# Kernel optimization log

Hardware: AMD Instinct MI355X
Metric: run time of the kernel (lower is better)

## Reference

```python
import jax, jax.numpy as jnp
import numpy as np

B, L, D, H = 4, 1024, 768, 12
HD = D // H  # head_dim = 64
SCALING = HD ** -0.5


def setup_inputs() -> dict:
    key = jax.random.key(0)
    ks = jax.random.split(key, 6)
    x = jax.random.normal(ks[0], (B, L, D), dtype=jnp.float32)
    attn_bias = jax.random.normal(ks[1], (B, H, L, L), dtype=jnp.float32)
    s_in = 1.0 / np.sqrt(D)
    w_in = jax.random.uniform(ks[2], (3 * D, D), dtype=jnp.float32, minval=-s_in, maxval=s_in)
    b_in = jax.random.uniform(ks[3], (3 * D,), dtype=jnp.float32, minval=-s_in, maxval=s_in)
    w_out = jax.random.uniform(ks[4], (D, D), dtype=jnp.float32, minval=-s_in, maxval=s_in)
    b_out = jax.random.uniform(ks[5], (D,), dtype=jnp.float32, minval=-s_in, maxval=s_in)
    return {"x": x, "attn_bias": attn_bias, "w_in": w_in, "b_in": b_in,
            "w_out": w_out, "b_out": b_out}


def reference(x, attn_bias, w_in, b_in, w_out, b_out):
    # fused QKV projection: [B, L, 3D]
    qkv = jnp.einsum('bld,ed->ble', x, w_in) + b_in
    q, k, v = jnp.split(qkv, 3, axis=-1)
    # [B, H, L, HD]
    q = q.reshape(B, L, H, HD).transpose(0, 2, 1, 3) * SCALING
    k = k.reshape(B, L, H, HD).transpose(0, 2, 1, 3)
    v = v.reshape(B, L, H, HD).transpose(0, 2, 1, 3)
    # bias-augmented attention scores: [B, H, L, L]
    scores = jnp.einsum('bhqd,bhkd->bhqk', q, k) + attn_bias
    probs = jax.nn.softmax(scores, axis=-1)
    # attend: [B, H, L, HD] -> [B, L, D]
    o = jnp.einsum('bhqk,bhkd->bhqd', probs, v)
    o = o.transpose(0, 2, 1, 3).reshape(B, L, D)
    return jnp.einsum('bld,ed->ble', o, w_out) + b_out
```

## Files before the change

### kernel.cpp

```cpp
#include <hip/hip_runtime.h>
#include <hip/hip_bf16.h>
#include <stdint.h>

#define B_ 4
#define L_ 1024
#define D_ 768
#define H_ 12
#define HD_ 64
#define M_ 4096
#define N3_ 2304

typedef float f32x4 __attribute__((ext_vector_type(4)));
typedef float f32x4v __attribute__((ext_vector_type(4)));
typedef short bf16x8 __attribute__((ext_vector_type(8)));
typedef unsigned short u16;
typedef u16 u16x8 __attribute__((ext_vector_type(8)));
typedef u16 u16x4 __attribute__((ext_vector_type(4)));

#define AS3 __attribute__((address_space(3)))
#define AS1 __attribute__((address_space(1)))

__device__ __forceinline__ void gll16(const void* g, void* l) {
  __builtin_amdgcn_global_load_lds((const AS1 void*)g, (AS3 void*)l, 16, 0, 0);
}

__device__ __forceinline__ u16 f2bf(float f) {
  uint32_t u = __builtin_bit_cast(uint32_t, f);
  u += 0x7fffu + ((u >> 16) & 1u);
  return (u16)(u >> 16);
}

__global__ void k_cvt3(const float* __restrict__ a, u16* __restrict__ ao, int na4,
                       const float* __restrict__ b, u16* __restrict__ bo, int nb4,
                       const float* __restrict__ c, u16* __restrict__ co, int nc4) {
  int i = blockIdx.x * 256 + threadIdx.x;
  const float* src;
  u16* dst;
  if (i < na4) {
    src = a; dst = ao;
  } else if (i < na4 + nb4) {
    src = b; dst = bo; i -= na4;
  } else if (i < na4 + nb4 + nc4) {
    src = c; dst = co; i -= na4 + nb4;
  } else {
    return;
  }
  f32x4v v = ((const f32x4v*)src)[i];
  u16x4 o;
  o.x = f2bf(v.x); o.y = f2bf(v.y); o.z = f2bf(v.z); o.w = f2bf(v.w);
  ((u16x4*)dst)[i] = o;
}

__global__ __launch_bounds__(256) void k_gemm_qkv(
    const u16* __restrict__ Xb, const u16* __restrict__ Wb,
    const float* __restrict__ b_in,
    u16* __restrict__ gQ, u16* __restrict__ gK, u16* __restrict__ gV) {
  __shared__ u16 As[128 * 64];
  __shared__ u16 Bs[128 * 64];
  const int tid = threadIdx.x;
  const int lane = tid & 63;
  const int w = tid >> 6;
  const int wm = (w >> 1) * 64;
  const int wn = (w & 1) * 64;
  const int lr = lane & 15;
  const int lg = lane >> 4;
  const int m0 = blockIdx.x * 128;
  const int n0 = blockIdx.y * 128;

  f32x4 acc[4][4];
#pragma unroll
  for (int i = 0; i < 4; ++i)
#pragma unroll
    for (int j = 0; j < 4; ++j) acc[i][j] = (f32x4){0.f, 0.f, 0.f, 0.f};

  for (int kt = 0; kt < 12; ++kt) {
    __syncthreads();
#pragma unroll
    for (int i = 0; i < 4; ++i) {
      int seg = i * 256 + tid;
      int row = seg >> 3;
      int sl = (seg & 7) ^ (row & 7);
      gll16(Xb + (size_t)(m0 + row) * 768 + kt * 64 + sl * 8, (char*)As + seg * 16);
      gll16(Wb + (size_t)(n0 + row) * 768 + kt * 64 + sl * 8, (char*)Bs + seg * 16);
    }
    __syncthreads();
#pragma unroll
    for (int kh = 0; kh < 2; ++kh) {
      bf16x8 af[4], bfr[4];
#pragma unroll
      for (int t = 0; t < 4; ++t) {
        int ra = wm + t * 16 + lr;
        af[t] = *(const bf16x8*)((const char*)As + ra * 128 +
                                 ((kh * 64 + lg * 16) ^ ((ra & 7) << 4)));
        int rb = wn + t * 16 + lr;
        bfr[t] = *(const bf16x8*)((const char*)Bs + rb * 128 +
                                  ((kh * 64 + lg * 16) ^ ((rb & 7) << 4)));
      }
#pragma unroll
      for (int mi = 0; mi < 4; ++mi)
#pragma unroll
        for (int ni = 0; ni < 4; ++ni)
          acc[mi][ni] = __builtin_amdgcn_mfma_f32_16x16x32_bf16(
              af[mi], bfr[ni], acc[mi][ni], 0, 0, 0);
    }
  }
  const int sec = blockIdx.y / 6;
  u16* dst = sec == 0 ? gQ : (sec == 1 ? gK : gV);
  const float scale = sec == 0 ? 0.125f : 1.0f;
#pragma unroll
  for (int ni = 0; ni < 4; ++ni) {
    int e = n0 + wn + ni * 16 + lr;
    float bias = b_in[e];
    int es = e - sec * 768;
    int h = es >> 6, d = es & 63;
#pragma unroll
    for (int mi = 0; mi < 4; ++mi) {
#pragma unroll
      for (int j = 0; j < 4; ++j) {
        int m = m0 + wm + mi * 16 + lg * 4 + j;
        int bb = m >> 10, lq = m & 1023;
        float vv = (acc[mi][ni][j] + bias) * scale;
        dst[(size_t)((bb * 12 + h) * 1024 + lq) * 64 + d] = f2bf(vv);
      }
    }
  }
}

__global__ __launch_bounds__(256) void k_transpose(const u16* __restrict__ V,
                                                   u16* __restrict__ Vt) {
  __shared__ u16 t[64][66];
  const int tid = threadIdx.x;
  const int bh = blockIdx.x >> 4;
  const int kv0 = (blockIdx.x & 15) * 64;
  {
    int r = tid >> 2, c0 = (tid & 3) * 16;
    const u16* src = V + (size_t)(bh * 1024 + kv0 + r) * 64 + c0;
#pragma unroll
    for (int p = 0; p < 2; ++p) {
      u16x8 x = *(const u16x8*)(src + p * 8);
#pragma unroll
      for (int e = 0; e < 8; ++e) t[r][c0 + p * 8 + e] = x[e];
    }
  }
  __syncthreads();
  {
    int d = tid >> 2, k0 = (tid & 3) * 16;
    u16* dst = Vt + (size_t)(bh * 64 + d) * 1024 + kv0 + k0;
#pragma unroll
    for (int p = 0; p < 2; ++p) {
      u16x8 o;
#pragma unroll
      for (int e = 0; e < 8; ++e) o[e] = t[k0 + p * 8 + e][d];
      *(u16x8*)(dst + p * 8) = o;
    }
  }
}

__global__ __launch_bounds__(256) void k_attn(
    const u16* __restrict__ gQ, const u16* __restrict__ gK,
    const u16* __restrict__ gVt, const float* __restrict__ gBias,
    u16* __restrict__ gO) {
  __shared__ u16 Ks[2][64 * 64];
  __shared__ u16 Vs[2][64 * 64];
  __shared__ u16 Pl[4][16 * 64];
  const int tid = threadIdx.x;
  const int lane = tid & 63;
  const int w = tid >> 6;
  const int lr = lane & 15;
  const int lg = lane >> 4;
  const int lb = (blockIdx.x & 7) * 96 + (blockIdx.x >> 3);
  const int bh = lb >> 4;
  const int q0 = (lb & 15) * 64;
  const int qr = q0 + w * 16;

#define STAGE_KV(buf, kv0)                                                         \
  do {                                                                             \
    _Pragma("unroll") for (int i_ = 0; i_ < 2; ++i_) {                             \
      int seg_ = i_ * 256 + tid;                                                   \
      int row_ = seg_ >> 3;                                                        \
      int sl_ = (seg_ & 7) ^ (row_ & 7);                                           \
      gll16(gK + (size_t)(bh * 1024 + (kv0) + row_) * 64 + sl_ * 8,                \
            (char*)Ks[buf] + seg_ * 16);                                           \
      gll16(gVt + (size_t)(bh * 64 + row_) * 1024 + (kv0) + sl_ * 8,               \
            (char*)Vs[buf] + seg_ * 16);                                           \
    }                                                                              \
  } while (0)

  bf16x8 qa[2];
#pragma unroll
  for (int kh = 0; kh < 2; ++kh)
    qa[kh] = *(const bf16x8*)(gQ + (size_t)(bh * 1024 + qr + lr) * 64 + kh * 32 + lg * 8);

  f32x4 oacc[4];
#pragma unroll
  for (int dt = 0; dt < 4; ++dt) oacc[dt] = (f32x4){0.f, 0.f, 0.f, 0.f};
  float mrow[4] = {-1e30f, -1e30f, -1e30f, -1e30f};
  float lrow[4] = {0.f, 0.f, 0.f, 0.f};

  const float* bbase = gBias + (size_t)(bh * 1024 + qr) * 1024;

  STAGE_KV(0, 0);
  float bcur[16];
#pragma unroll
  for (int ni = 0; ni < 4; ++ni)
#pragma unroll
    for (int j = 0; j < 4; ++j)
      bcur[ni * 4 + j] = __builtin_nontemporal_load(
          bbase + (size_t)(lg * 4 + j) * 1024 + ni * 16 + lr);
  __syncthreads();

  for (int t = 0; t < 16; ++t) {
    const int cur = t & 1;
    if (t < 15) STAGE_KV(cur ^ 1, (t + 1) * 64);

    f32x4 s[4];
#pragma unroll
    for (int ni = 0; ni < 4; ++ni) s[ni] = (f32x4){0.f, 0.f, 0.f, 0.f};
    __builtin_amdgcn_s_setprio(1);
#pragma unroll
    for (int kh = 0; kh < 2; ++kh) {
#pragma unroll
      for (int ni = 0; ni < 4; ++ni) {
        int rb = ni * 16 + lr;
        bf16x8 kb = *(const bf16x8*)((const char*)Ks[cur] + rb * 128 +
                                     ((kh * 64 + lg * 16) ^ ((rb & 7) << 4)));
        s[ni] = __builtin_amdgcn_mfma_f32_16x16x32_bf16(qa[kh], kb, s[ni], 0, 0, 0);
      }
    }
    __builtin_amdgcn_s_setprio(0);

#pragma unroll
    for (int ni = 0; ni < 4; ++ni)
#pragma unroll
      for (int j = 0; j < 4; ++j) s[ni][j] += bcur[ni * 4 + j];

    float bnx[16];
    if (t < 15) {
      const float* bp = bbase + (t + 1) * 64;
#pragma unroll
      for (int ni = 0; ni < 4; ++ni)
#pragma unroll
        for (int j = 0; j < 4; ++j)
          bnx[ni * 4 + j] = __builtin_nontemporal_load(
              bp + (size_t)(lg * 4 + j) * 1024 + ni * 16 + lr);
    }

#pragma unroll
    for (int j = 0; j < 4; ++j) {
      float vm = fmaxf(fmaxf(s[0][j], s[1][j]), fmaxf(s[2][j], s[3][j]));
      vm = fmaxf(vm, __shfl_xor(vm, 1));
      vm = fmaxf(vm, __shfl_xor(vm, 2));
      vm = fmaxf(vm, __shfl_xor(vm, 4));
      vm = fmaxf(vm, __shfl_xor(vm, 8));
      float mnew = fmaxf(mrow[j], vm);
      float al = __expf(mrow[j] - mnew);
      mrow[j] = mnew;
      float rs = 0.f;
#pragma unroll
      for (int ni = 0; ni < 4; ++ni) {
        float p = __expf(s[ni][j] - mnew);
        s[ni][j] = p;
        rs += p;
      }
      rs += __shfl_xor(rs, 1);
      rs += __shfl_xor(rs, 2);
      rs += __shfl_xor(rs, 4);
      rs += __shfl_xor(rs, 8);
      lrow[j] = lrow[j] * al + rs;
#pragma unroll
      for (int dt = 0; dt < 4; ++dt) oacc[dt][j] *= al;
    }

    u16* pw = Pl[w];
#pragma unroll
    for (int ni = 0; ni < 4; ++ni)
#pragma unroll
      for (int j = 0; j < 4; ++j) {
        int row = lg * 4 + j;
        int bc = (ni * 16 + lr) * 2;
        *(u16*)((char*)pw + row * 128 + (bc ^ ((row & 7) << 4))) = f2bf(s[ni][j]);
      }
    __builtin_amdgcn_s_setprio(1);
#pragma unroll
    for (int kh = 0; kh < 2; ++kh) {
      bf16x8 pa = *(const bf16x8*)((const char*)pw + lr * 128 +
                                   ((kh * 64 + lg * 16) ^ ((lr & 7) << 4)));
#pragma unroll
      for (int dt = 0; dt < 4; ++dt) {
        int rv = dt * 16 + lr;
        bf16x8 vb = *(const bf16x8*)((const char*)Vs[cur] + rv * 128 +
                                     ((kh * 64 + lg * 16) ^ ((rv & 7) << 4)));
        oacc[dt] = __builtin_amdgcn_mfma_f32_16x16x32_bf16(pa, vb, oacc[dt], 0, 0, 0);
      }
    }
    __builtin_amdgcn_s_setprio(0);

    if (t < 15) {
#pragma unroll
      for (int z = 0; z < 16; ++z) bcur[z] = bnx[z];
    }
    __syncthreads();
  }

  const int bg = bh / 12, h = bh % 12;
#pragma unroll
  for (int j = 0; j < 4; ++j) {
    float inv = 1.0f / lrow[j];
    int row = qr + lg * 4 + j;
#pragma unroll
    for (int dt = 0; dt < 4; ++dt) {
      gO[(size_t)(bg * 1024 + row) * 768 + h * 64 + dt * 16 + lr] =
          f2bf(oacc[dt][j] * inv);
    }
  }
#undef STAGE_KV
}

__global__ __launch_bounds__(256) void k_gemm_out(
    const u16* __restrict__ Ob, const u16* __restrict__ Wb,
    const float* __restrict__ b_out, float* __restrict__ out) {
  __shared__ u16 As[128 * 64];
  __shared__ u16 Bs[128 * 64];
  const int tid = threadIdx.x;
  const int lane = tid & 63;
  const int w = tid >> 6;
  const int wm = (w >> 1) * 64;
  const int wn = (w & 1) * 64;
  const int lr = lane & 15;
  const int lg = lane >> 4;
  const int m0 = blockIdx.x * 128;
  const int n0 = blockIdx.y * 128;

  f32x4 acc[4][4];
#pragma unroll
  for (int i = 0; i < 4; ++i)
#pragma unroll
    for (int j = 0; j < 4; ++j) acc[i][j] = (f32x4){0.f, 0.f, 0.f, 0.f};

  for (int kt = 0; kt < 12; ++kt) {
    __syncthreads();
#pragma unroll
    for (int i = 0; i < 4; ++i) {
      int seg = i * 256 + tid;
      int row = seg >> 3;
      int sl = (seg & 7) ^ (row & 7);
      gll16(Ob + (size_t)(m0 + row) * 768 + kt * 64 + sl * 8, (char*)As + seg * 16);
      gll16(Wb + (size_t)(n0 + row) * 768 + kt * 64 + sl * 8, (char*)Bs + seg * 16);
    }
    __syncthreads();
#pragma unroll
    for (int kh = 0; kh < 2; ++kh) {
      bf16x8 af[4], bfr[4];
#pragma unroll
      for (int t = 0; t < 4; ++t) {
        int ra = wm + t * 16 + lr;
        af[t] = *(const bf16x8*)((const char*)As + ra * 128 +
                                 ((kh * 64 + lg * 16) ^ ((ra & 7) << 4)));
        int rb = wn + t * 16 + lr;
        bfr[t] = *(const bf16x8*)((const char*)Bs + rb * 128 +
                                  ((kh * 64 + lg * 16) ^ ((rb & 7) << 4)));
      }
#pragma unroll
      for (int mi = 0; mi < 4; ++mi)
#pragma unroll
        for (int ni = 0; ni < 4; ++ni)
          acc[mi][ni] = __builtin_amdgcn_mfma_f32_16x16x32_bf16(
              af[mi], bfr[ni], acc[mi][ni], 0, 0, 0);
    }
  }
#pragma unroll
  for (int ni = 0; ni < 4; ++ni) {
    int n = n0 + wn + ni * 16 + lr;
    float bias = b_out[n];
#pragma unroll
    for (int mi = 0; mi < 4; ++mi) {
#pragma unroll
      for (int j = 0; j < 4; ++j) {
        int m = m0 + wm + mi * 16 + lg * 4 + j;
        out[(size_t)m * 768 + n] = acc[mi][ni][j] + bias;
      }
    }
  }
}

extern "C" void kernel_launch(void* const* d_in, const int* in_sizes, int n_in,
                              void* d_out, int out_size, void* d_ws, size_t ws_size,
                              hipStream_t stream) {
  const float* x = (const float*)d_in[0];
  const float* attn_bias = (const float*)d_in[1];
  const float* w_in = (const float*)d_in[2];
  const float* b_in = (const float*)d_in[3];
  const float* w_out = (const float*)d_in[4];
  const float* b_out = (const float*)d_in[5];
  float* out = (float*)d_out;

  char* ws = (char*)d_ws;
  size_t off = 0;
  u16* xb = (u16*)(ws + off);  off += (size_t)M_ * D_ * 2;
  u16* wib = (u16*)(ws + off); off += (size_t)N3_ * D_ * 2;
  u16* wob = (u16*)(ws + off); off += (size_t)D_ * D_ * 2;
  u16* q = (u16*)(ws + off);   off += (size_t)48 * 1024 * 64 * 2;
  u16* k = (u16*)(ws + off);   off += (size_t)48 * 1024 * 64 * 2;
  u16* v = (u16*)(ws + off);   off += (size_t)48 * 1024 * 64 * 2;
  u16* vt = (u16*)(ws + off);  off += (size_t)48 * 1024 * 64 * 2;
  u16* ob = (u16*)(ws + off);  off += (size_t)M_ * D_ * 2;

  const int na4 = (M_ * D_) / 4;
  const int nb4 = (N3_ * D_) / 4;
  const int nc4 = (D_ * D_) / 4;
  k_cvt3<<<(na4 + nb4 + nc4 + 255) / 256, 256, 0, stream>>>(
      x, xb, na4, w_in, wib, nb4, w_out, wob, nc4);
  k_gemm_qkv<<<dim3(32, 18), 256, 0, stream>>>(xb, wib, b_in, q, k, v);
  k_transpose<<<768, 256, 0, stream>>>(v, vt);
  k_attn<<<768, 256, 0, stream>>>(q, k, vt, attn_bias, ob);
  k_gemm_out<<<dim3(32, 6), 256, 0, stream>>>(ob, wob, b_out, out);
}
```

Measured before the change: 130.0 us.

## Stage attention bias in LDS, read K/V directly into registers, shrink out-proj tiles

The attention kernel no longer stages K and V through shared memory. Each wave loads its K and V fragments straight from global memory into registers, and the bias tile is instead double-buffered into LDS with async global-to-LDS loads and a swizzle. The QK^T MFMA operands are swapped so each lane owns a single query row, which turns the per-row max and sum reductions into two cross-group shuffles and lets P be written to LDS as packed 32-bit stores. The output projection GEMM moves from 128x128 to 64x64 tiles to launch four times as many blocks. The costs are redundant per-wave K/V global loads, since four waves now read the same K/V tile, and lower arithmetic intensity in the output GEMM.

```diff
diff --git a/kernel.cpp b/kernel.cpp
--- a/kernel.cpp
+++ b/kernel.cpp
@@ -16,6 +16,7 @@
 typedef unsigned short u16;
 typedef u16 u16x8 __attribute__((ext_vector_type(8)));
 typedef u16 u16x4 __attribute__((ext_vector_type(4)));
+typedef uint32_t u32x2 __attribute__((ext_vector_type(2)));
 
 #define AS3 __attribute__((address_space(3)))
 #define AS1 __attribute__((address_space(1)))
@@ -160,9 +161,8 @@
     const u16* __restrict__ gQ, const u16* __restrict__ gK,
     const u16* __restrict__ gVt, const float* __restrict__ gBias,
     u16* __restrict__ gO) {
-  __shared__ u16 Ks[2][64 * 64];
-  __shared__ u16 Vs[2][64 * 64];
-  __shared__ u16 Pl[4][16 * 64];
+  __shared__ f32x4 biasS[2][1024];
+  __shared__ f32x4 PlV[4][128];
   const int tid = threadIdx.x;
   const int lane = tid & 63;
   const int w = tid >> 6;
@@ -173,17 +173,15 @@
   const int q0 = (lb & 15) * 64;
   const int qr = q0 + w * 16;
 
-#define STAGE_KV(buf, kv0)                                                         \
-  do {                                                                             \
-    _Pragma("unroll") for (int i_ = 0; i_ < 2; ++i_) {                             \
-      int seg_ = i_ * 256 + tid;                                                   \
-      int row_ = seg_ >> 3;                                                        \
-      int sl_ = (seg_ & 7) ^ (row_ & 7);                                           \
-      gll16(gK + (size_t)(bh * 1024 + (kv0) + row_) * 64 + sl_ * 8,                \
-            (char*)Ks[buf] + seg_ * 16);                                           \
-      gll16(gVt + (size_t)(bh * 64 + row_) * 1024 + (kv0) + sl_ * 8,               \
-            (char*)Vs[buf] + seg_ * 16);                                           \
-    }                                                                              \
+#define STAGE_BIAS(buf, kv0)                                                  \
+  do {                                                                        \
+    _Pragma("unroll") for (int i_ = 0; i_ < 4; ++i_) {                        \
+      int seg_ = i_ * 256 + tid;                                              \
+      int qrow_ = seg_ >> 4;                                                  \
+      int c_ = (seg_ & 15) ^ (qrow_ & 7);                                     \
+      gll16(gBias + (size_t)(bh * 1024 + q0 + qrow_) * 1024 + (kv0) + c_ * 4, \
+            (char*)biasS + (buf) * 16384 + seg_ * 16);                        \
+    }                                                                         \
   } while (0)
 
   bf16x8 qa[2];
@@ -194,153 +192,144 @@
   f32x4 oacc[4];
 #pragma unroll
   for (int dt = 0; dt < 4; ++dt) oacc[dt] = (f32x4){0.f, 0.f, 0.f, 0.f};
-  float mrow[4] = {-1e30f, -1e30f, -1e30f, -1e30f};
-  float lrow[4] = {0.f, 0.f, 0.f, 0.f};
-
-  const float* bbase = gBias + (size_t)(bh * 1024 + qr) * 1024;
-
-  STAGE_KV(0, 0);
-  float bcur[16];
-#pragma unroll
-  for (int ni = 0; ni < 4; ++ni)
-#pragma unroll
-    for (int j = 0; j < 4; ++j)
-      bcur[ni * 4 + j] = __builtin_nontemporal_load(
-          bbase + (size_t)(lg * 4 + j) * 1024 + ni * 16 + lr);
+  float mrow = -1e30f, lrow = 0.f;
+
+  STAGE_BIAS(0, 0);
   __syncthreads();
+
+  char* plw = (char*)PlV[w];
+  const int swz = (lr & 7) << 4;
 
   for (int t = 0; t < 16; ++t) {
     const int cur = t & 1;
-    if (t < 15) STAGE_KV(cur ^ 1, (t + 1) * 64);
+    const int kv0 = t * 64;
+
+    bf16x8 kb[2][4];
+#pragma unroll
+    for (int kh = 0; kh < 2; ++kh)
+#pragma unroll
+      for (int ni = 0; ni < 4; ++ni)
+        kb[kh][ni] = *(const bf16x8*)(
+            gK + ((size_t)(bh * 1024 + kv0 + ni * 16 + lr) << 6) + kh * 32 + lg * 8);
+    bf16x8 vb[2][4];
+#pragma unroll
+    for (int kh = 0; kh < 2; ++kh)
+#pragma unroll
+      for (int dt = 0; dt < 4; ++dt)
+        vb[kh][dt] = *(const bf16x8*)(
+            gVt + ((size_t)(bh * 64 + dt * 16 + lr) << 10) + kv0 + kh * 32 + lg * 8);
+
+    if (t < 15) STAGE_BIAS(cur ^ 1, kv0 + 64);
 
     f32x4 s[4];
 #pragma unroll
     for (int ni = 0; ni < 4; ++ni) s[ni] = (f32x4){0.f, 0.f, 0.f, 0.f};
     __builtin_amdgcn_s_setprio(1);
 #pragma unroll
+    for (int kh = 0; kh < 2; ++kh)
+#pragma unroll
+      for (int ni = 0; ni < 4; ++ni)
+        s[ni] = __builtin_amdgcn_mfma_f32_16x16x32_bf16(kb[kh][ni], qa[kh], s[ni], 0, 0, 0);
+    __builtin_amdgcn_s_setprio(0);
+
+#pragma unroll
+    for (int ni = 0; ni < 4; ++ni) {
+      f32x4 bv = *(const f32x4*)((const char*)biasS + cur * 16384 +
+                                 (w * 16 + lr) * 256 + (((ni * 4 + lg) ^ (lr & 7)) << 4));
+      s[ni] += bv;
+    }
+
+    float mx0 = fmaxf(fmaxf(s[0][0], s[0][1]), fmaxf(s[0][2], s[0][3]));
+    float mx1 = fmaxf(fmaxf(s[1][0], s[1][1]), fmaxf(s[1][2], s[1][3]));
+    float mx2 = fmaxf(fmaxf(s[2][0], s[2][1]), fmaxf(s[2][2], s[2][3]));
+    float mx3 = fmaxf(fmaxf(s[3][0], s[3][1]), fmaxf(s[3][2], s[3][3]));
+    float vmax = fmaxf(fmaxf(mx0, mx1), fmaxf(mx2, mx3));
+    vmax = fmaxf(vmax, __shfl_xor(vmax, 16));
+    vmax = fmaxf(vmax, __shfl_xor(vmax, 32));
+    float mnew = fmaxf(mrow, vmax);
+    float al = __expf(mrow - mnew);
+    mrow = mnew;
+#pragma unroll
+    for (int ni = 0; ni < 4; ++ni)
+#pragma unroll
+      for (int j = 0; j < 4; ++j) s[ni][j] = __expf(s[ni][j] - mnew);
+    float r0 = (s[0][0] + s[0][1]) + (s[0][2] + s[0][3]);
+    float r1 = (s[1][0] + s[1][1]) + (s[1][2] + s[1][3]);
+    float r2 = (s[2][0] + s[2][1]) + (s[2][2] + s[2][3]);
+    float r3 = (s[3][0] + s[3][1]) + (s[3][2] + s[3][3]);
+    float rs = (r0 + r1) + (r2 + r3);
+    rs += __shfl_xor(rs, 16);
+    rs += __shfl_xor(rs, 32);
+    lrow = lrow * al + rs;
+
+    f32x4 av;
+#pragma unroll
+    for (int j = 0; j < 4; ++j) av[j] = __shfl(al, (lane & 48) | (lg * 4 + j));
+#pragma unroll
+    for (int dt = 0; dt < 4; ++dt) oacc[dt] *= av;
+
+#pragma unroll
+    for (int ni = 0; ni < 4; ++ni) {
+      uint32_t w0 = (uint32_t)f2bf(s[ni][0]) | ((uint32_t)f2bf(s[ni][1]) << 16);
+      uint32_t w1 = (uint32_t)f2bf(s[ni][2]) | ((uint32_t)f2bf(s[ni][3]) << 16);
+      u32x2 pv = {w0, w1};
+      *(u32x2*)(plw + lr * 128 + ((ni * 32 + lg * 8) ^ swz)) = pv;
+    }
+    __builtin_amdgcn_s_setprio(1);
+#pragma unroll
     for (int kh = 0; kh < 2; ++kh) {
-#pragma unroll
-      for (int ni = 0; ni < 4; ++ni) {
-        int rb = ni * 16 + lr;
-        bf16x8 kb = *(const bf16x8*)((const char*)Ks[cur] + rb * 128 +
-                                     ((kh * 64 + lg * 16) ^ ((rb & 7) << 4)));
-        s[ni] = __builtin_amdgcn_mfma_f32_16x16x32_bf16(qa[kh], kb, s[ni], 0, 0, 0);
-      }
+      bf16x8 pa = *(const bf16x8*)(plw + lr * 128 + ((kh * 64 + lg * 16) ^ swz));
+#pragma unroll
+      for (int dt = 0; dt < 4; ++dt)
+        oacc[dt] = __builtin_amdgcn_mfma_f32_16x16x32_bf16(pa, vb[kh][dt], oacc[dt], 0, 0, 0);
     }
     __builtin_amdgcn_s_setprio(0);
 
-#pragma unroll
-    for (int ni = 0; ni < 4; ++ni)
-#pragma unroll
-      for (int j = 0; j < 4; ++j) s[ni][j] += bcur[ni * 4 + j];
-
-    float bnx[16];
-    if (t < 15) {
-      const float* bp = bbase + (t + 1) * 64;
-#pragma unroll
-      for (int ni = 0; ni < 4; ++ni)
-#pragma unroll
-        for (int j = 0; j < 4; ++j)
-          bnx[ni * 4 + j] = __builtin_nontemporal_load(
-              bp + (size_t)(lg * 4 + j) * 1024 + ni * 16 + lr);
-    }
-
-#pragma unroll
-    for (int j = 0; j < 4; ++j) {
-      float vm = fmaxf(fmaxf(s[0][j], s[1][j]), fmaxf(s[2][j], s[3][j]));
-      vm = fmaxf(vm, __shfl_xor(vm, 1));
-      vm = fmaxf(vm, __shfl_xor(vm, 2));
-      vm = fmaxf(vm, __shfl_xor(vm, 4));
-      vm = fmaxf(vm, __shfl_xor(vm, 8));
-      float mnew = fmaxf(mrow[j], vm);
-      float al = __expf(mrow[j] - mnew);
-      mrow[j] = mnew;
-      float rs = 0.f;
-#pragma unroll
-      for (int ni = 0; ni < 4; ++ni) {
-        float p = __expf(s[ni][j] - mnew);
-        s[ni][j] = p;
-        rs += p;
-      }
-      rs += __shfl_xor(rs, 1);
-      rs += __shfl_xor(rs, 2);
-      rs += __shfl_xor(rs, 4);
-      rs += __shfl_xor(rs, 8);
-      lrow[j] = lrow[j] * al + rs;
-#pragma unroll
-      for (int dt = 0; dt < 4; ++dt) oacc[dt][j] *= al;
-    }
-
-    u16* pw = Pl[w];
-#pragma unroll
-    for (int ni = 0; ni < 4; ++ni)
-#pragma unroll
-      for (int j = 0; j < 4; ++j) {
-        int row = lg * 4 + j;
-        int bc = (ni * 16 + lr) * 2;
-        *(u16*)((char*)pw + row * 128 + (bc ^ ((row & 7) << 4))) = f2bf(s[ni][j]);
-      }
-    __builtin_amdgcn_s_setprio(1);
-#pragma unroll
-    for (int kh = 0; kh < 2; ++kh) {
-      bf16x8 pa = *(const bf16x8*)((const char*)pw + lr * 128 +
-                                   ((kh * 64 + lg * 16) ^ ((lr & 7) << 4)));
-#pragma unroll
-      for (int dt = 0; dt < 4; ++dt) {
-        int rv = dt * 16 + lr;
-        bf16x8 vb = *(const bf16x8*)((const char*)Vs[cur] + rv * 128 +
-                                     ((kh * 64 + lg * 16) ^ ((rv & 7) << 4)));
-        oacc[dt] = __builtin_amdgcn_mfma_f32_16x16x32_bf16(pa, vb, oacc[dt], 0, 0, 0);
-      }
-    }
-    __builtin_amdgcn_s_setprio(0);
-
-    if (t < 15) {
-#pragma unroll
-      for (int z = 0; z < 16; ++z) bcur[z] = bnx[z];
-    }
     __syncthreads();
   }
 
+  float inv = 1.0f / lrow;
+  f32x4 iv;
+#pragma unroll
+  for (int j = 0; j < 4; ++j) iv[j] = __shfl(inv, (lane & 48) | (lg * 4 + j));
   const int bg = bh / 12, h = bh % 12;
 #pragma unroll
   for (int j = 0; j < 4; ++j) {
-    float inv = 1.0f / lrow[j];
     int row = qr + lg * 4 + j;
 #pragma unroll
     for (int dt = 0; dt < 4; ++dt) {
       gO[(size_t)(bg * 1024 + row) * 768 + h * 64 + dt * 16 + lr] =
-          f2bf(oacc[dt][j] * inv);
-    }
-  }
-#undef STAGE_KV
+          f2bf(oacc[dt][j] * iv[j]);
+    }
+  }
+#undef STAGE_BIAS
 }
 
 __global__ __launch_bounds__(256) void k_gemm_out(
     const u16* __restrict__ Ob, const u16* __restrict__ Wb,
     const float* __restrict__ b_out, float* __restrict__ out) {
-  __shared__ u16 As[128 * 64];
-  __shared__ u16 Bs[128 * 64];
+  __shared__ u16 As[64 * 64];
+  __shared__ u16 Bs[64 * 64];
   const int tid = threadIdx.x;
   const int lane = tid & 63;
   const int w = tid >> 6;
-  const int wm = (w >> 1) * 64;
-  const int wn = (w & 1) * 64;
+  const int wm = (w >> 1) * 32;
+  const int wn = (w & 1) * 32;
   const int lr = lane & 15;
   const int lg = lane >> 4;
-  const int m0 = blockIdx.x * 128;
-  const int n0 = blockIdx.y * 128;
-
-  f32x4 acc[4][4];
-#pragma unroll
-  for (int i = 0; i < 4; ++i)
-#pragma unroll
-    for (int j = 0; j < 4; ++j) acc[i][j] = (f32x4){0.f, 0.f, 0.f, 0.f};
+  const int m0 = blockIdx.x * 64;
+  const int n0 = blockIdx.y * 64;
+
+  f32x4 acc[2][2];
+#pragma unroll
+  for (int i = 0; i < 2; ++i)
+#pragma unroll
+    for (int j = 0; j < 2; ++j) acc[i][j] = (f32x4){0.f, 0.f, 0.f, 0.f};
 
   for (int kt = 0; kt < 12; ++kt) {
     __syncthreads();
 #pragma unroll
-    for (int i = 0; i < 4; ++i) {
+    for (int i = 0; i < 2; ++i) {
       int seg = i * 256 + tid;
       int row = seg >> 3;
       int sl = (seg & 7) ^ (row & 7);
@@ -350,9 +339,9 @@
     __syncthreads();
 #pragma unroll
     for (int kh = 0; kh < 2; ++kh) {
-      bf16x8 af[4], bfr[4];
-#pragma unroll
-      for (int t = 0; t < 4; ++t) {
+      bf16x8 af[2], bfr[2];
+#pragma unroll
+      for (int t = 0; t < 2; ++t) {
         int ra = wm + t * 16 + lr;
         af[t] = *(const bf16x8*)((const char*)As + ra * 128 +
                                  ((kh * 64 + lg * 16) ^ ((ra & 7) << 4)));
@@ -361,19 +350,19 @@
                                   ((kh * 64 + lg * 16) ^ ((rb & 7) << 4)));
       }
 #pragma unroll
-      for (int mi = 0; mi < 4; ++mi)
-#pragma unroll
-        for (int ni = 0; ni < 4; ++ni)
+      for (int mi = 0; mi < 2; ++mi)
+#pragma unroll
+        for (int ni = 0; ni < 2; ++ni)
           acc[mi][ni] = __builtin_amdgcn_mfma_f32_16x16x32_bf16(
               af[mi], bfr[ni], acc[mi][ni], 0, 0, 0);
     }
   }
 #pragma unroll
-  for (int ni = 0; ni < 4; ++ni) {
+  for (int ni = 0; ni < 2; ++ni) {
     int n = n0 + wn + ni * 16 + lr;
     float bias = b_out[n];
 #pragma unroll
-    for (int mi = 0; mi < 4; ++mi) {
+    for (int mi = 0; mi < 2; ++mi) {
 #pragma unroll
       for (int j = 0; j < 4; ++j) {
         int m = m0 + wm + mi * 16 + lg * 4 + j;
@@ -413,5 +402,5 @@
   k_gemm_qkv<<<dim3(32, 18), 256, 0, stream>>>(xb, wib, b_in, q, k, v);
   k_transpose<<<768, 256, 0, stream>>>(v, vt);
   k_attn<<<768, 256, 0, stream>>>(q, k, vt, attn_bias, ob);
-  k_gemm_out<<<dim3(32, 6), 256, 0, stream>>>(ob, wob, b_out, out);
-}
+  k_gemm_out<<<dim3(64, 12), 256, 0, stream>>>(ob, wob, b_out, out);
+}
```

Result: slower. 161.5 us (+24.2%).
